# Performance work log

Measured on AMD Instinct MI355X. Metric: run time of the kernel, lower is better.

Reference implementation:

```python
import jax, jax.numpy as jnp
import numpy as np

C = 256  # in_channels
B, N = 8, 2048


def setup_inputs() -> dict:
    key = jax.random.key(0)
    ks = jax.random.split(key, 9)
    s = 1.0 / np.sqrt(C)  # conv1d default init scale (approx)
    return {
        "x": jax.random.normal(ks[0], (B, C, N), jnp.float32),
        "wq": jax.random.normal(ks[1], (C, C), jnp.float32) * s,
        "bq": jax.random.normal(ks[2], (C,), jnp.float32) * s,
        "wk": jax.random.normal(ks[3], (C, C), jnp.float32) * s,
        "bk": jax.random.normal(ks[4], (C,), jnp.float32) * s,
        "wv": jax.random.normal(ks[5], (C, C), jnp.float32) * s,
        "bv": jax.random.normal(ks[6], (C,), jnp.float32) * s,
        "wo": jax.random.normal(ks[7], (C, C), jnp.float32) * s,
        "bo": jax.random.normal(ks[8], (C,), jnp.float32) * s,
    }


def reference(x, wq, bq, wk, bk, wv, bv, wo, bo):
    # 1x1 Conv1d == channel-wise linear: [C_out,C_in] x [B,C_in,N] -> [B,C_out,N]
    proj = lambda w, b, t: jnp.einsum('ci,bin->bcn', w, t) + b[None, :, None]
    q = proj(wq, bq, x)
    k = proj(wk, bk, x)
    v = proj(wv, bv, x)
    norm = 1.0 / (x.shape[1] ** 0.5)
    # scores: w[b,n,m] = sum_c q[b,c,n] k[b,c,m]
    w = jnp.einsum('bcn,bcm->bnm', q, k) * norm
    w = jax.nn.softmax(w, axis=2)
    # attn output: sum_m v[b,c,m] w[b,n,m] -> [B,C,N]
    av = jnp.einsum('bcm,bnm->bcn', v, w)
    out = proj(wo, bo, av)
    return x + out
```

## Files before the change

kernel.cpp:

```cpp
#include <hip/hip_runtime.h>
#include <hip/hip_bf16.h>

#define CCH 256
#define NSEQ 2048
#define BATCH 8

typedef __hip_bfloat16 bf16;
typedef short s8v __attribute__((ext_vector_type(8)));
typedef float f4v __attribute__((ext_vector_type(4)));
typedef float f16v __attribute__((ext_vector_type(16)));

struct __align__(8) bf16x4 { bf16 v[4]; };

__device__ __forceinline__ float b2f(bf16 h) { return __bfloat162float(h); }
__device__ __forceinline__ bf16 f2b(float f) { return __float2bfloat16(f); }

#define MFMA16(a, b, c) __builtin_amdgcn_mfma_f32_16x16x32_bf16((a), (b), (c), 0, 0, 0)
#define MFMA32(a, b, c) __builtin_amdgcn_mfma_f32_32x32x16_bf16((a), (b), (c), 0, 0, 0)

__device__ __forceinline__ void gload_lds16(const bf16* g, bf16* l) {
    __builtin_amdgcn_global_load_lds(
        (const __attribute__((address_space(1))) unsigned int*)(g),
        (__attribute__((address_space(3))) unsigned int*)(l), 16, 0, 0);
}

__global__ __launch_bounds__(256) void prepw_kernel(
    const float* __restrict__ wq, const float* __restrict__ wk,
    const float* __restrict__ wv,
    bf16* __restrict__ wqb, bf16* __restrict__ wkb, bf16* __restrict__ wvb)
{
    int base = (blockIdx.x * 256 + threadIdx.x) * 8;
    int mat = base >> 16, off = base & 65535;
    const float* s = (mat == 0) ? wq : (mat == 1) ? wk : wv;
    bf16* d       = (mat == 0) ? wqb : (mat == 1) ? wkb : wvb;
    #pragma unroll
    for (int j = 0; j < 8; ++j) d[off + j] = f2b(s[off + j]);
}

__global__ __launch_bounds__(512, 4) void qkvprep_kernel(
    const float* __restrict__ x,
    const bf16* __restrict__ Wq, const bf16* __restrict__ Wk,
    const bf16* __restrict__ Wv,
    const float* __restrict__ bq, const float* __restrict__ bk,
    const float* __restrict__ bv,
    bf16* __restrict__ qTt, bf16* __restrict__ kTt, bf16* __restrict__ Vt)
{
    __shared__ bf16 xs[64][260];

    const int tile = blockIdx.x;
    const int flat0 = tile * 64;
    const int phase = blockIdx.y;
    const int b = flat0 >> 11, nn = flat0 & 2047;
    const int tid = threadIdx.x;
    const int w = tid >> 6, lane = tid & 63;
    const int l15 = lane & 15, quad = lane >> 4;
    const int ng = w & 3;
    const int ch = w >> 2;
    const float* xb = x + (size_t)b * CCH * NSEQ;

    #pragma unroll
    for (int i = 0; i < 8; ++i) {
        int f4i = i * 512 + tid;
        int c = f4i >> 4, nq = f4i & 15;
        float4 v4 = *(const float4*)&xb[(size_t)c * NSEQ + nn + nq * 4];
        xs[nq * 4 + 0][c] = f2b(v4.x);
        xs[nq * 4 + 1][c] = f2b(v4.y);
        xs[nq * 4 + 2][c] = f2b(v4.z);
        xs[nq * 4 + 3][c] = f2b(v4.w);
    }
    __syncthreads();

    s8v xf[8];
    #pragma unroll
    for (int t = 0; t < 8; ++t)
        xf[t] = *(const s8v*)&xs[ng * 16 + l15][t * 32 + quad * 8];

    bf16* qt = qTt + (size_t)tile * 16384;
    bf16* kt = kTt + (size_t)tile * 16384;

    if (phase == 0) {
        #pragma unroll 2
        for (int i = 0; i < 8; ++i) {
            int cs = ch * 8 + i;
            const s8v* wr = (const s8v*)(Wq + (size_t)(cs * 16 + l15) * CCH);
            f4v a0 = {}, a1 = {};
            #pragma unroll
            for (int t = 0; t < 4; ++t) {
                a0 = MFMA16(xf[t], wr[t * 4 + quad], a0);
                a1 = MFMA16(xf[t + 4], wr[(t + 4) * 4 + quad], a1);
            }
            int c = cs * 16 + l15;
            float bb = bq[c];
            #pragma unroll
            for (int r = 0; r < 4; ++r) {
                int nl = ng * 16 + quad * 4 + r;
                qt[(c >> 3) * 512 + nl * 8 + (c & 7)] = f2b((a0[r] + a1[r] + bb) * 0.0625f);
            }
        }
        #pragma unroll 2
        for (int i = 0; i < 4; ++i) {
            int cs = ch * 4 + i;
            const s8v* wr = (const s8v*)(Wk + (size_t)(cs * 16 + l15) * CCH);
            f4v a0 = {}, a1 = {};
            #pragma unroll
            for (int t = 0; t < 4; ++t) {
                a0 = MFMA16(xf[t], wr[t * 4 + quad], a0);
                a1 = MFMA16(xf[t + 4], wr[(t + 4) * 4 + quad], a1);
            }
            int c = cs * 16 + l15;
            float bb = bk[c];
            #pragma unroll
            for (int r = 0; r < 4; ++r) {
                int nl = ng * 16 + quad * 4 + r;
                kt[(c >> 3) * 512 + nl * 8 + (c & 7)] = f2b(a0[r] + a1[r] + bb);
            }
        }
    } else {
        bf16* Vtb = Vt + (size_t)b * CCH * NSEQ;
        const int nb = nn + ng * 16 + l15;
        const size_t vbase = (size_t)(nb >> 5) * 8192 + (nb & 31);
        #pragma unroll 2
        for (int i = 0; i < 8; ++i) {
            int cs = ch * 8 + i;
            const s8v* wr = (const s8v*)(Wv + (size_t)(cs * 16 + l15) * CCH);
            f4v a0 = {}, a1 = {};
            #pragma unroll
            for (int t = 0; t < 4; ++t) {
                a0 = MFMA16(wr[t * 4 + quad], xf[t], a0);
                a1 = MFMA16(wr[(t + 4) * 4 + quad], xf[t + 4], a1);
            }
            #pragma unroll
            for (int r = 0; r < 4; ++r) {
                int c = cs * 16 + quad * 4 + r;
                Vtb[vbase + (size_t)c * 32] = f2b(a0[r] + a1[r] + bv[c]);
            }
        }
        #pragma unroll 2
        for (int i = 0; i < 4; ++i) {
            int cs = 8 + ch * 4 + i;
            const s8v* wr = (const s8v*)(Wk + (size_t)(cs * 16 + l15) * CCH);
            f4v a0 = {}, a1 = {};
            #pragma unroll
            for (int t = 0; t < 4; ++t) {
                a0 = MFMA16(xf[t], wr[t * 4 + quad], a0);
                a1 = MFMA16(xf[t + 4], wr[(t + 4) * 4 + quad], a1);
            }
            int c = cs * 16 + l15;
            float bb = bk[c];
            #pragma unroll
            for (int r = 0; r < 4; ++r) {
                int nl = ng * 16 + quad * 4 + r;
                kt[(c >> 3) * 512 + nl * 8 + (c & 7)] = f2b(a0[r] + a1[r] + bb);
            }
        }
    }
}

__global__ __launch_bounds__(256, 2) void flash_kernel(
    const bf16* __restrict__ qTt, const bf16* __restrict__ kTt,
    const bf16* __restrict__ Vt, bf16* __restrict__ Opart,
    float* __restrict__ lpart)
{
    __shared__ bf16 Kc[16384];
    __shared__ bf16 Ps[64][68];
    __shared__ float l_s[2][64];

    const int b = blockIdx.x, nt = blockIdx.y, ms = blockIdx.z;
    const int tid = threadIdx.x;
    const int W = tid >> 6, lane = tid & 63;
    const int l31 = lane & 31, h = lane >> 5;
    const int ng = W >> 1, mg = W & 1;
    const int mb = ms * 16;
    const bf16* Vtb = Vt + (size_t)b * CCH * NSEQ;

    s8v qf[16];
    {
        const bf16* qt = qTt + (size_t)(b * 32 + nt) * 16384;
        #pragma unroll
        for (int t = 0; t < 16; ++t)
            qf[t] = *(const s8v*)&qt[(t * 2 + h) * 512 + (ng * 32 + l31) * 8];
    }
    const bf16* vrow[2];
    #pragma unroll
    for (int cr = 0; cr < 2; ++cr)
        vrow[cr] = Vtb + (size_t)(W * 64 + cr * 32 + l31) * 32 + h * 8;

    f16v O[2][2] = {};
    float lacc[16] = {};

    {
        const bf16* kt = kTt + (size_t)(b * 32 + mb) * 16384;
        #pragma unroll
        for (int i = 0; i < 8; ++i) {
            int ch = W * 8 + i;
            gload_lds16(kt + ch * 512 + lane * 8, &Kc[ch * 512]);
        }
    }
    __syncthreads();

    for (int mt = 0; mt < 16; ++mt) {
        f16v S0 = {}, S1 = {};
        #pragma unroll
        for (int t = 0; t < 8; ++t) {
            s8v kf0 = *(const s8v*)&Kc[(t * 2 + h) * 512 + (mg * 32 + l31) * 8];
            s8v kf1 = *(const s8v*)&Kc[((t + 8) * 2 + h) * 512 + (mg * 32 + l31) * 8];
            S0 = MFMA32(qf[t], kf0, S0);
            S1 = MFMA32(qf[t + 8], kf1, S1);
        }
        s8v vf[2][4];
        #pragma unroll
        for (int ks = 0; ks < 4; ++ks)
            #pragma unroll
            for (int cr = 0; cr < 2; ++cr)
                vf[cr][ks] = *(const s8v*)(vrow[cr]
                    + (size_t)((mb + mt) * 2 + (ks >> 1)) * 8192
                    + (ks & 1) * 16);
        #pragma unroll
        for (int reg = 0; reg < 16; ++reg) {
            float e = __expf(fminf(S0[reg] + S1[reg], 60.f));
            lacc[reg] += e;
            int row = (reg & 3) + 8 * (reg >> 2) + 4 * h;
            Ps[ng * 32 + row][mg * 32 + l31] = f2b(e);
        }
        __syncthreads();

        if (mt < 15) {
            const bf16* kt = kTt + (size_t)(b * 32 + mb + mt + 1) * 16384;
            #pragma unroll
            for (int i = 0; i < 8; ++i) {
                int ch = W * 8 + i;
                gload_lds16(kt + ch * 512 + lane * 8, &Kc[ch * 512]);
            }
        }
        #pragma unroll
        for (int ks = 0; ks < 4; ++ks) {
            s8v pf0 = *(const s8v*)&Ps[l31][ks * 16 + h * 8];
            s8v pf1 = *(const s8v*)&Ps[32 + l31][ks * 16 + h * 8];
            O[0][0] = MFMA32(vf[0][ks], pf0, O[0][0]);
            O[0][1] = MFMA32(vf[0][ks], pf1, O[0][1]);
            O[1][0] = MFMA32(vf[1][ks], pf0, O[1][0]);
            O[1][1] = MFMA32(vf[1][ks], pf1, O[1][1]);
        }
        __syncthreads();
    }

    #pragma unroll
    for (int reg = 0; reg < 16; ++reg) {
        float s = lacc[reg];
        #pragma unroll
        for (int off = 1; off < 32; off <<= 1) s += __shfl_xor(s, off);
        lacc[reg] = s;
    }
    if (l31 == 0) {
        #pragma unroll
        for (int reg = 0; reg < 16; ++reg) {
            int row = (reg & 3) + 8 * (reg >> 2) + 4 * h;
            l_s[mg][ng * 32 + row] = lacc[reg];
        }
    }
    __syncthreads();
    const size_t pb = (size_t)(b * 32 + nt) * 2 + ms;
    if (tid < 64) lpart[pb * 64 + tid] = l_s[0][tid] + l_s[1][tid];

    bf16* Ob = Opart + pb * 16384;
    #pragma unroll
    for (int cr = 0; cr < 2; ++cr)
        #pragma unroll
        for (int g2 = 0; g2 < 2; ++g2) {
            int n = g2 * 32 + l31;
            #pragma unroll
            for (int q2 = 0; q2 < 4; ++q2) {
                bf16x4 pk;
                #pragma unroll
                for (int j = 0; j < 4; ++j) pk.v[j] = f2b(O[cr][g2][q2 * 4 + j]);
                int c = W * 64 + cr * 32 + q2 * 8 + 4 * h;
                *(bf16x4*)&Ob[(size_t)n * 256 + c] = pk;
            }
        }
}

__global__ __launch_bounds__(256, 2) void outproj_kernel(
    const bf16* __restrict__ Opart, const float* __restrict__ lpart,
    const float* __restrict__ Wo, const float* __restrict__ bo,
    const float* __restrict__ x, float* __restrict__ out)
{
    __shared__ bf16 avs[64][260];
    __shared__ float ils[64];

    const int bx = blockIdx.x;
    const int flat0 = bx * 64;
    const int c0 = blockIdx.y * 128;
    const int tid = threadIdx.x;
    const int w = tid >> 6, lane = tid & 63;
    const int l15 = lane & 15, quad = lane >> 4;

    if (tid < 64)
        ils[tid] = 1.f / (lpart[(size_t)(bx * 2) * 64 + tid]
                        + lpart[(size_t)(bx * 2 + 1) * 64 + tid]);
    __syncthreads();

    const bf16x4* O0 = (const bf16x4*)(Opart + (size_t)(bx * 2) * 16384);
    const bf16x4* O1 = O0 + 4096;
    #pragma unroll
    for (int i = 0; i < 16; ++i) {
        int u = i * 256 + tid;
        int n = u >> 6;
        bf16x4 a = O0[u], bb = O1[u];
        float il = ils[n];
        bf16x4 o;
        #pragma unroll
        for (int t = 0; t < 4; ++t)
            o.v[t] = f2b((b2f(a.v[t]) + b2f(bb.v[t])) * il);
        *(bf16x4*)&avs[n][(u & 63) * 4] = o;
    }
    __syncthreads();

    const int bidx = flat0 >> 11, nn = flat0 & 2047;
    const size_t base = (size_t)bidx * CCH * NSEQ;

    for (int g = 0; g < 2; ++g) {
        const int cg = c0 + g * 64 + w * 16;
        s8v af[8];
        #pragma unroll
        for (int t = 0; t < 8; ++t) {
            const float* wp = Wo + (size_t)(cg + l15) * CCH + t * 32 + quad * 8;
            float4 f0 = *(const float4*)wp;
            float4 f1 = *(const float4*)(wp + 4);
            bf16 a8[8] = { f2b(f0.x), f2b(f0.y), f2b(f0.z), f2b(f0.w),
                           f2b(f1.x), f2b(f1.y), f2b(f1.z), f2b(f1.w) };
            af[t] = *(const s8v*)a8;
        }
        f4v O[4] = {};
        #pragma unroll
        for (int nt = 0; nt < 4; ++nt)
            #pragma unroll
            for (int t = 0; t < 8; ++t) {
                s8v br = *(const s8v*)&avs[nt * 16 + l15][t * 32 + quad * 8];
                O[nt] = MFMA16(af[t], br, O[nt]);
            }
        #pragma unroll
        for (int r = 0; r < 4; ++r) {
            int c = cg + quad * 4 + r;
            float bb = bo[c];
            #pragma unroll
            for (int nt = 0; nt < 4; ++nt) {
                size_t idx = base + (size_t)c * NSEQ + nn + nt * 16 + l15;
                out[idx] = O[nt][r] + bb + x[idx];
            }
        }
    }
}

extern "C" void kernel_launch(void* const* d_in, const int* in_sizes, int n_in,
                              void* d_out, int out_size, void* d_ws, size_t ws_size,
                              hipStream_t stream) {
    (void)in_sizes; (void)n_in; (void)out_size; (void)ws_size;
    const float* x  = (const float*)d_in[0];
    const float* wq = (const float*)d_in[1];
    const float* bq = (const float*)d_in[2];
    const float* wk = (const float*)d_in[3];
    const float* bk = (const float*)d_in[4];
    const float* wv = (const float*)d_in[5];
    const float* bv = (const float*)d_in[6];
    const float* wo = (const float*)d_in[7];
    const float* bo = (const float*)d_in[8];
    float* out = (float*)d_out;

    const size_t T = (size_t)BATCH * CCH * NSEQ;
    bf16* qTt  = (bf16*)d_ws;
    bf16* kTt  = qTt + T;
    bf16* Vt   = kTt + T;
    bf16* wqb  = Vt + T;
    bf16* wkb  = wqb + 65536;
    bf16* wvb  = wkb + 65536;
    float* lpart = (float*)(wvb + 65536);
    bf16* Opart  = (bf16*)(lpart + 32768);

    prepw_kernel<<<96, 256, 0, stream>>>(wq, wk, wv, wqb, wkb, wvb);
    qkvprep_kernel<<<dim3(256, 2), 512, 0, stream>>>(
        x, wqb, wkb, wvb, bq, bk, bv, qTt, kTt, Vt);
    flash_kernel<<<dim3(8, 32, 2), 256, 0, stream>>>(qTt, kTt, Vt, Opart, lpart);
    outproj_kernel<<<dim3(256, 2), 256, 0, stream>>>(Opart, lpart, wo, bo, x, out);
}
```

Before: 190.7 us.

## Stage QKV weights through double-buffered swizzled LDS and vectorize projection stores

The prep kernel now writes bf16 weights in an XOR-swizzled layout. The QKV projection kernel double-buffers 16-row weight chunks into LDS using async global_load_lds, instead of having every wave read weights directly from global memory. The MFMA operand order is swapped for Q/K so each lane writes four contiguous bf16 outputs, and V stores are packed the same way, replacing scattered 2-byte stores. This adds a __syncthreads per chunk and extra LDS use, which may lower occupancy.

```diff
diff --git a/kernel.cpp b/kernel.cpp
--- a/kernel.cpp
+++ b/kernel.cpp
@@ -33,8 +33,11 @@
     int mat = base >> 16, off = base & 65535;
     const float* s = (mat == 0) ? wq : (mat == 1) ? wk : wv;
     bf16* d       = (mat == 0) ? wqb : (mat == 1) ? wkb : wvb;
-    #pragma unroll
-    for (int j = 0; j < 8; ++j) d[off + j] = f2b(s[off + j]);
+    int doff = off ^ (((off >> 8) & 7) << 3);
+    bf16 tmp[8];
+    #pragma unroll
+    for (int j = 0; j < 8; ++j) tmp[j] = f2b(s[off + j]);
+    *(s8v*)&d[doff] = *(const s8v*)tmp;
 }
 
 __global__ __launch_bounds__(512, 4) void qkvprep_kernel(
@@ -46,6 +49,7 @@
     bf16* __restrict__ qTt, bf16* __restrict__ kTt, bf16* __restrict__ Vt)
 {
     __shared__ bf16 xs[64][260];
+    __shared__ bf16 wbuf[2][2][4096];
 
     const int tile = blockIdx.x;
     const int flat0 = tile * 64;
@@ -58,6 +62,27 @@
     const int ch = w >> 2;
     const float* xb = x + (size_t)b * CCH * NSEQ;
 
+    bf16* qt = qTt + (size_t)tile * 16384;
+    bf16* kt = kTt + (size_t)tile * 16384;
+    bf16* Vtb = Vt + (size_t)b * CCH * NSEQ;
+
+    auto chunk_ptr = [&](int j) -> const bf16* {
+        if (phase == 0)
+            return (j < 8) ? Wq + (size_t)(ch * 8 + j) * 4096
+                           : Wk + (size_t)(ch * 4 + (j - 8)) * 4096;
+        else
+            return (j < 8) ? Wv + (size_t)(ch * 8 + j) * 4096
+                           : Wk + (size_t)(8 + ch * 4 + (j - 8)) * 4096;
+    };
+    auto stage = [&](int j, int par) {
+        const bf16* src = chunk_ptr(j);
+        bf16* dst = &wbuf[ch][par][0];
+        int seg = (w & 3) * 2;
+        gload_lds16(src + (seg + 0) * 512 + lane * 8, dst + (seg + 0) * 512);
+        gload_lds16(src + (seg + 1) * 512 + lane * 8, dst + (seg + 1) * 512);
+    };
+
+    stage(0, 0);
     #pragma unroll
     for (int i = 0; i < 8; ++i) {
         int f4i = i * 512 + tid;
@@ -75,84 +100,59 @@
     for (int t = 0; t < 8; ++t)
         xf[t] = *(const s8v*)&xs[ng * 16 + l15][t * 32 + quad * 8];
 
-    bf16* qt = qTt + (size_t)tile * 16384;
-    bf16* kt = kTt + (size_t)tile * 16384;
-
-    if (phase == 0) {
-        #pragma unroll 2
-        for (int i = 0; i < 8; ++i) {
-            int cs = ch * 8 + i;
-            const s8v* wr = (const s8v*)(Wq + (size_t)(cs * 16 + l15) * CCH);
+    int par = 0;
+    #pragma unroll
+    for (int j = 0; j < 12; ++j) {
+        if (j < 11) stage(j + 1, par ^ 1);
+
+        const char* wb = (const char*)&wbuf[ch][par][0];
+        s8v wf[8];
+        #pragma unroll
+        for (int t = 0; t < 8; ++t)
+            wf[t] = *(const s8v*)(wb + l15 * 512 +
+                                  ((t * 64 + quad * 16) ^ ((l15 & 7) << 4)));
+
+        if (phase == 0 || j >= 8) {
             f4v a0 = {}, a1 = {};
             #pragma unroll
             for (int t = 0; t < 4; ++t) {
-                a0 = MFMA16(xf[t], wr[t * 4 + quad], a0);
-                a1 = MFMA16(xf[t + 4], wr[(t + 4) * 4 + quad], a1);
-            }
+                a0 = MFMA16(wf[t], xf[t], a0);
+                a1 = MFMA16(wf[t + 4], xf[t + 4], a1);
+            }
+            const bool isq = (phase == 0) && (j < 8);
+            const int cs = (phase == 0)
+                ? (j < 8 ? ch * 8 + j : ch * 4 + (j - 8))
+                : (8 + ch * 4 + (j - 8));
+            const float* bm = isq ? bq : bk;
+            bf16* ot = isq ? qt : kt;
+            const float sc = isq ? 0.0625f : 1.0f;
+            float4 bb4 = *(const float4*)&bm[cs * 16 + quad * 4];
+            float bbr[4] = { bb4.x, bb4.y, bb4.z, bb4.w };
+            bf16x4 pk;
+            #pragma unroll
+            for (int r = 0; r < 4; ++r)
+                pk.v[r] = f2b((a0[r] + a1[r] + bbr[r]) * sc);
+            int nl = ng * 16 + l15;
+            *(bf16x4*)&ot[(cs * 2 + (quad >> 1)) * 512 + nl * 8 + (quad & 1) * 4] = pk;
+        } else {
+            f4v a0 = {}, a1 = {};
+            #pragma unroll
+            for (int t = 0; t < 4; ++t) {
+                a0 = MFMA16(xf[t], wf[t], a0);
+                a1 = MFMA16(xf[t + 4], wf[t + 4], a1);
+            }
+            const int cs = ch * 8 + j;
             int c = cs * 16 + l15;
-            float bb = bq[c];
-            #pragma unroll
-            for (int r = 0; r < 4; ++r) {
-                int nl = ng * 16 + quad * 4 + r;
-                qt[(c >> 3) * 512 + nl * 8 + (c & 7)] = f2b((a0[r] + a1[r] + bb) * 0.0625f);
-            }
-        }
-        #pragma unroll 2
-        for (int i = 0; i < 4; ++i) {
-            int cs = ch * 4 + i;
-            const s8v* wr = (const s8v*)(Wk + (size_t)(cs * 16 + l15) * CCH);
-            f4v a0 = {}, a1 = {};
-            #pragma unroll
-            for (int t = 0; t < 4; ++t) {
-                a0 = MFMA16(xf[t], wr[t * 4 + quad], a0);
-                a1 = MFMA16(xf[t + 4], wr[(t + 4) * 4 + quad], a1);
-            }
-            int c = cs * 16 + l15;
-            float bb = bk[c];
-            #pragma unroll
-            for (int r = 0; r < 4; ++r) {
-                int nl = ng * 16 + quad * 4 + r;
-                kt[(c >> 3) * 512 + nl * 8 + (c & 7)] = f2b(a0[r] + a1[r] + bb);
-            }
-        }
-    } else {
-        bf16* Vtb = Vt + (size_t)b * CCH * NSEQ;
-        const int nb = nn + ng * 16 + l15;
-        const size_t vbase = (size_t)(nb >> 5) * 8192 + (nb & 31);
-        #pragma unroll 2
-        for (int i = 0; i < 8; ++i) {
-            int cs = ch * 8 + i;
-            const s8v* wr = (const s8v*)(Wv + (size_t)(cs * 16 + l15) * CCH);
-            f4v a0 = {}, a1 = {};
-            #pragma unroll
-            for (int t = 0; t < 4; ++t) {
-                a0 = MFMA16(wr[t * 4 + quad], xf[t], a0);
-                a1 = MFMA16(wr[(t + 4) * 4 + quad], xf[t + 4], a1);
-            }
-            #pragma unroll
-            for (int r = 0; r < 4; ++r) {
-                int c = cs * 16 + quad * 4 + r;
-                Vtb[vbase + (size_t)c * 32] = f2b(a0[r] + a1[r] + bv[c]);
-            }
-        }
-        #pragma unroll 2
-        for (int i = 0; i < 4; ++i) {
-            int cs = 8 + ch * 4 + i;
-            const s8v* wr = (const s8v*)(Wk + (size_t)(cs * 16 + l15) * CCH);
-            f4v a0 = {}, a1 = {};
-            #pragma unroll
-            for (int t = 0; t < 4; ++t) {
-                a0 = MFMA16(xf[t], wr[t * 4 + quad], a0);
-                a1 = MFMA16(xf[t + 4], wr[(t + 4) * 4 + quad], a1);
-            }
-            int c = cs * 16 + l15;
-            float bb = bk[c];
-            #pragma unroll
-            for (int r = 0; r < 4; ++r) {
-                int nl = ng * 16 + quad * 4 + r;
-                kt[(c >> 3) * 512 + nl * 8 + (c & 7)] = f2b(a0[r] + a1[r] + bb);
-            }
-        }
+            float bb = bv[c];
+            int nb0 = nn + ng * 16 + quad * 4;
+            bf16x4 pk;
+            #pragma unroll
+            for (int r = 0; r < 4; ++r)
+                pk.v[r] = f2b(a0[r] + a1[r] + bb);
+            *(bf16x4*)&Vtb[(size_t)(nb0 >> 5) * 8192 + (size_t)c * 32 + (nb0 & 31)] = pk;
+        }
+        __syncthreads();
+        par ^= 1;
     }
 }
 
```

After: 162.6 us. -14.7%, faster.
